# Performance work log

Hardware: AMD Instinct MI355X
Metric: run time of the kernel (lower is better)

## Reference

```python
import jax, jax.numpy as jnp
import numpy as np

FOCAL = 555.555
CROP_SIZE = 5
CROP_STEP = CROP_SIZE // 2  # 2
PADDING = CROP_SIZE        # 5
N_VIEWS = 16
IMG_SIZE = 400
N_POINTS = 65536


def _make_poses(n, radius=4.0, elev=-0.5):
    """NeRF-style camera-to-world matrices looking at the origin."""
    poses = []
    up = np.array([0.0, 0.0, 1.0], np.float64)
    for i in range(n):
        theta = 2.0 * np.pi * i / n
        eye = radius * np.array([np.cos(theta) * np.cos(elev),
                                 np.sin(theta) * np.cos(elev),
                                 np.sin(elev)], np.float64)
        z = eye / np.linalg.norm(eye)
        x = np.cross(up, z); x /= np.linalg.norm(x)
        y = np.cross(z, x)
        c2w = np.eye(4, dtype=np.float64)
        c2w[:3, 0] = x; c2w[:3, 1] = y; c2w[:3, 2] = z; c2w[:3, 3] = eye
        poses.append(c2w)
    return np.stack(poses).astype(np.float32)


def setup_inputs() -> dict:
    key = jax.random.key(0)
    k1, k2 = jax.random.split(key)
    points = jax.random.normal(k1, (N_POINTS, 3), jnp.float32)          # world pts near origin
    images = jax.random.uniform(k2, (N_VIEWS, IMG_SIZE, IMG_SIZE, 3), jnp.float32)
    poses = jnp.asarray(_make_poses(N_VIEWS))                            # [N,4,4]
    return {"points": points, "images": images, "poses": poses}


def _forward(points, images, poses):
    N, size = images.shape[0], images.shape[1]
    Hp = size + 2 * PADDING  # padded image side (grid normalized by this)
    dt = points.dtype

    # --- init-time camera setup (pose flip + inverse, intrinsics) ---
    flip = jnp.diag(jnp.array([-1.0, 1.0, 1.0, 1.0], dt))
    M = jnp.linalg.inv(poses @ flip)[:, :3, :]                           # [N,3,4] world->cam
    K = jnp.array([[FOCAL, 0.0, 0.5 * size],
                   [0.0, FOCAL, 0.5 * size],
                   [0.0, 0.0, 1.0]], dt)
    imgs = jnp.transpose(images, (0, 3, 1, 2))                           # [N,C,H,W]
    imgs = jnp.pad(imgs, ((0, 0), (0, 0), (PADDING, PADDING), (PADDING, PADDING)))  # zeros

    # --- projection ---
    P = points.shape[0]
    pts = jnp.concatenate([points, jnp.ones((P, 1), dt)], axis=1)        # [P,4]
    ps = jnp.einsum('ij,njk,pk->nip', K, M, pts)                         # [N,3,P]
    pix = jnp.clip((ps[:, :2] / ps[:, 2][:, None]) / size, 0.0, 1.0)     # [N,2,P] in [0,1]
    coord_norm = jnp.transpose(pix * 2.0 - 1.0, (0, 2, 1))               # [N,P,2]
    pixels = jnp.transpose(pix * size, (0, 2, 1))                        # [N,P,2] pixel units

    # --- 5x5 patch grid in padded-image pixel coords ---
    x = pixels[..., 0] + PADDING - CROP_STEP                             # [N,P]
    y = pixels[..., 1] + PADDING - CROP_STEP
    offs = jnp.arange(CROP_SIZE, dtype=dt)
    scale = (Hp - 1) / Hp  # grid_sample align_corners=True after v/Hp*2-1 normalization
    # NOTE: original stacks grid=[all_y, all_x, 0]: grid_sample x-coord (width) = all_y,
    # y-coord (height) = all_x. Rows vary along patch dim i, cols along patch dim j.
    rows = (x[:, :, None, None] + offs[None, None, :, None]) * scale     # [N,P,5,5]
    cols = (y[:, :, None, None] + offs[None, None, None, :]) * scale     # [N,P,5,5]

    def sample_view(img, r, c):  # img [C,Hp,Hp]; r,c [P,5,5]; bilinear, zeros padding
        r0f = jnp.floor(r); c0f = jnp.floor(c)
        wr = r - r0f; wc = c - c0f
        r0 = r0f.astype(jnp.int32); c0 = c0f.astype(jnp.int32)

        def gather(ri, ci):
            valid = ((ri >= 0) & (ri < Hp) & (ci >= 0) & (ci < Hp)).astype(img.dtype)
            v = img[:, jnp.clip(ri, 0, Hp - 1), jnp.clip(ci, 0, Hp - 1)]  # [C,P,5,5]
            return v * valid

        return (gather(r0, c0) * (1 - wr) * (1 - wc)
                + gather(r0, c0 + 1) * (1 - wr) * wc
                + gather(r0 + 1, c0) * wr * (1 - wc)
                + gather(r0 + 1, c0 + 1) * wr * wc)

    feats = jax.vmap(sample_view)(imgs, rows, cols)                      # [N,C,P,5,5]
    feats = jnp.transpose(feats, (2, 0, 1, 3, 4))                        # [P,N,C,5,5]
    return feats, coord_norm


def reference(points, images, poses):
    # Returns (feats [P,N,3,5,5], coord_norm [N,P,2]) -- the two tensors fed to the
    # external transformer in the original module.
    return _forward(points, images, poses)
```

## Files before the change

kernel.cpp:

```cpp
#include <hip/hip_runtime.h>

constexpr int   NPTS   = 65536;
constexpr int   NVIEWS = 16;
constexpr int   SZ     = 400;
constexpr int   PAD    = 5;
constexpr float FOCAL  = 555.555f;
constexpr float SCALE  = 409.0f / 410.0f;

constexpr long long FEATS_N = (long long)NPTS * NVIEWS * 3 * 25;

typedef float vfloat2 __attribute__((ext_vector_type(2)));

__global__ void setup_km(const float* __restrict__ poses, float* __restrict__ km) {
    int n = threadIdx.x;
    if (n >= NVIEWS) return;
    const float* A = poses + n * 16;
    float x0 = A[0], x1 = A[4], x2 = A[8];
    float y0 = A[1], y1 = A[5], y2 = A[9];
    float z0 = A[2], z1 = A[6], z2 = A[10];
    float t0 = A[3], t1 = A[7], t2 = A[11];

    float M0[4] = { -x0, -x1, -x2,  (x0 * t0 + x1 * t1 + x2 * t2) };
    float M1[4] = {  y0,  y1,  y2, -(y0 * t0 + y1 * t1 + y2 * t2) };
    float M2[4] = {  z0,  z1,  z2, -(z0 * t0 + z1 * t1 + z2 * t2) };

    const float f = FOCAL, cx = 0.5f * SZ;
    float* o = km + n * 12;
#pragma unroll
    for (int k = 0; k < 4; ++k) o[k]     = f * M0[k] + cx * M2[k];
#pragma unroll
    for (int k = 0; k < 4; ++k) o[4 + k] = f * M1[k] + cx * M2[k];
#pragma unroll
    for (int k = 0; k < 4; ++k) o[8 + k] = M2[k];
}

__device__ __forceinline__ void fetch3(const float* __restrict__ ib, int r, int c,
                                       float& a, float& b, float& d) {
    bool ok = ((unsigned)r < (unsigned)SZ) & ((unsigned)c < (unsigned)SZ);
    int rc = min(max(r, 0), SZ - 1);
    int cc = min(max(c, 0), SZ - 1);
    const float* q = ib + ((long long)rc * SZ + cc) * 3;
    float m = ok ? 1.0f : 0.0f;
    a = q[0] * m;
    b = q[1] * m;
    d = q[2] * m;
}

__global__ __launch_bounds__(256) void feats_kernel(const float* __restrict__ pts,
                                                    const float* __restrict__ imgs,
                                                    const float* __restrict__ km,
                                                    float* __restrict__ out) {
    unsigned b   = blockIdx.x;
    unsigned n   = (b & 7u) + 8u * ((b >> 3) & 1u);
    unsigned idx = (b >> 4) * 256u + threadIdx.x;
    unsigned p   = idx / 25u;
    unsigned ij  = idx % 25u;

    float px = pts[3 * p], py = pts[3 * p + 1], pz = pts[3 * p + 2];
    const float* k = km + n * 12;
    float psx = k[0] * px + k[1] * py + k[2]  * pz + k[3];
    float psy = k[4] * px + k[5] * py + k[6]  * pz + k[7];
    float psz = k[8] * px + k[9] * py + k[10] * pz + k[11];
    float inv = __builtin_amdgcn_rcpf(psz);
    float u = psx * inv * (1.0f / SZ);
    float v = psy * inv * (1.0f / SZ);
    u = fminf(fmaxf(u, 0.0f), 1.0f);
    v = fminf(fmaxf(v, 0.0f), 1.0f);
    float x = u * SZ + (float)(PAD - 2);
    float y = v * SZ + (float)(PAD - 2);

    int i = (int)(ij / 5u);
    int j = (int)(ij % 5u);

    float r  = (x + (float)i) * SCALE;
    float cc = (y + (float)j) * SCALE;
    float r0f = floorf(r);
    float c0f = floorf(cc);
    float wr = r - r0f;
    float wc = cc - c0f;
    int r0 = (int)r0f - PAD;
    int c0 = (int)c0f - PAD;

    const float* ib = imgs + (long long)n * (SZ * SZ * 3);
    float a00, b00, d00, a01, b01, d01, a10, b10, d10, a11, b11, d11;
    fetch3(ib, r0,     c0,     a00, b00, d00);
    fetch3(ib, r0,     c0 + 1, a01, b01, d01);
    fetch3(ib, r0 + 1, c0,     a10, b10, d10);
    fetch3(ib, r0 + 1, c0 + 1, a11, b11, d11);

    float w00 = (1.0f - wr) * (1.0f - wc);
    float w01 = (1.0f - wr) * wc;
    float w10 = wr * (1.0f - wc);
    float w11 = wr * wc;

    float o0 = w00 * a00 + w01 * a01 + w10 * a10 + w11 * a11;
    float o1 = w00 * b00 + w01 * b01 + w10 * b10 + w11 * b11;
    float o2 = w00 * d00 + w01 * d01 + w10 * d10 + w11 * d11;

    unsigned pn = p * 16u + n;
    float* ob = out + (long long)pn * 75 + ij;
    __builtin_nontemporal_store(o0, &ob[0]);
    __builtin_nontemporal_store(o1, &ob[25]);
    __builtin_nontemporal_store(o2, &ob[50]);
}

__global__ __launch_bounds__(256) void coord_kernel(const float* __restrict__ pts,
                                                    const float* __restrict__ km,
                                                    float* __restrict__ out2) {
    unsigned tid = blockIdx.x * 256u + threadIdx.x;
    unsigned p = tid & (NPTS - 1);
    unsigned n = tid >> 16;

    float px = pts[3 * p], py = pts[3 * p + 1], pz = pts[3 * p + 2];
    const float* k = km + n * 12;
    float psx = k[0] * px + k[1] * py + k[2]  * pz + k[3];
    float psy = k[4] * px + k[5] * py + k[6]  * pz + k[7];
    float psz = k[8] * px + k[9] * py + k[10] * pz + k[11];
    float inv = __builtin_amdgcn_rcpf(psz);
    float u = psx * inv * (1.0f / SZ);
    float v = psy * inv * (1.0f / SZ);
    u = fminf(fmaxf(u, 0.0f), 1.0f);
    v = fminf(fmaxf(v, 0.0f), 1.0f);

    vfloat2* o = (vfloat2*)out2;
    vfloat2 val = { 2.0f * u - 1.0f, 2.0f * v - 1.0f };
    __builtin_nontemporal_store(val, &o[tid]);
}

extern "C" void kernel_launch(void* const* d_in, const int* in_sizes, int n_in,
                              void* d_out, int out_size, void* d_ws, size_t ws_size,
                              hipStream_t stream) {
    const float* points = (const float*)d_in[0];
    const float* images = (const float*)d_in[1];
    const float* poses  = (const float*)d_in[2];
    float* out = (float*)d_out;
    float* km  = (float*)d_ws;

    setup_km<<<1, 64, 0, stream>>>(poses, km);

    feats_kernel<<<102400, 256, 0, stream>>>(points, images, km, out);

    coord_kernel<<<4096, 256, 0, stream>>>(points, km, out + FEATS_N);
}
```

Before: 433.0 us.

## Pre-pad images and stage per-point 6x6 patch in LDS for bilinear sampling

Adds a kernel that writes zero-padded copies of the images (row pitch 412) to workspace. The feats kernel now gives each 32-lane group one (point, view) pair: the group loads the covering 6-row patch into shared memory with float4 loads, then 25 lanes do the bilinear taps from LDS without bounds checks. This removes the per-tap clamping and scattered 4-byte global gathers. In exchange it adds a full image-padding pass, launches more blocks, leaves 7 of 32 lanes idle in the compute phase, and adds a block-wide barrier. The old path is kept as a fallback when the workspace is too small.

```diff
diff --git a/kernel.cpp b/kernel.cpp
--- a/kernel.cpp
+++ b/kernel.cpp
@@ -4,10 +4,14 @@
 constexpr int   NVIEWS = 16;
 constexpr int   SZ     = 400;
 constexpr int   PAD    = 5;
+constexpr int   HP     = 410;
+constexpr int   WP     = 412;
 constexpr float FOCAL  = 555.555f;
 constexpr float SCALE  = 409.0f / 410.0f;
 
 constexpr long long FEATS_N = (long long)NPTS * NVIEWS * 3 * 25;
+constexpr int PADIMG_FLOATS = NVIEWS * HP * WP * 3;
+constexpr int ROWB = WP * 3 * 4;
 
 typedef float vfloat2 __attribute__((ext_vector_type(2)));
 
@@ -34,27 +38,36 @@
     for (int k = 0; k < 4; ++k) o[8 + k] = M2[k];
 }
 
-__device__ __forceinline__ void fetch3(const float* __restrict__ ib, int r, int c,
-                                       float& a, float& b, float& d) {
-    bool ok = ((unsigned)r < (unsigned)SZ) & ((unsigned)c < (unsigned)SZ);
-    int rc = min(max(r, 0), SZ - 1);
-    int cc = min(max(c, 0), SZ - 1);
-    const float* q = ib + ((long long)rc * SZ + cc) * 3;
-    float m = ok ? 1.0f : 0.0f;
-    a = q[0] * m;
-    b = q[1] * m;
-    d = q[2] * m;
-}
-
-__global__ __launch_bounds__(256) void feats_kernel(const float* __restrict__ pts,
-                                                    const float* __restrict__ imgs,
-                                                    const float* __restrict__ km,
-                                                    float* __restrict__ out) {
-    unsigned b   = blockIdx.x;
-    unsigned n   = (b & 7u) + 8u * ((b >> 3) & 1u);
-    unsigned idx = (b >> 4) * 256u + threadIdx.x;
-    unsigned p   = idx / 25u;
-    unsigned ij  = idx % 25u;
+__global__ __launch_bounds__(256) void pad_kernel(const float* __restrict__ images,
+                                                  float* __restrict__ dst) {
+    unsigned idx = blockIdx.x * 256u + threadIdx.x;
+    constexpr unsigned TOT = (unsigned)NVIEWS * HP * WP;
+    if (idx >= TOT) return;
+    unsigned n   = idx / (unsigned)(HP * WP);
+    unsigned rem = idx - n * (unsigned)(HP * WP);
+    unsigned rr  = rem / (unsigned)WP;
+    unsigned cc  = rem - rr * (unsigned)WP;
+    float a = 0.0f, b = 0.0f, c = 0.0f;
+    int r = (int)rr - PAD, q = (int)cc - PAD;
+    if (r >= 0 && r < SZ && q >= 0 && q < SZ) {
+        const float* s = images + (((long long)n * SZ + r) * SZ + q) * 3;
+        a = s[0]; b = s[1]; c = s[2];
+    }
+    float* d = dst + (long long)idx * 3;
+    d[0] = a; d[1] = b; d[2] = c;
+}
+
+__global__ __launch_bounds__(256) void feats_coop(const float* __restrict__ pts,
+                                                  const float* __restrict__ imgpad,
+                                                  const float* __restrict__ km,
+                                                  float* __restrict__ out) {
+    __shared__ float lds[8 * 168];
+
+    unsigned b = blockIdx.x;
+    unsigned n = (b & 7u) + 8u * ((b >> 3) & 1u);
+    unsigned g = threadIdx.x >> 5;
+    unsigned l = threadIdx.x & 31u;
+    unsigned p = (b >> 4) * 8u + g;
 
     float px = pts[3 * p], py = pts[3 * p + 1], pz = pts[3 * p + 2];
     const float* k = km + n * 12;
@@ -69,47 +82,92 @@
     float x = u * SZ + (float)(PAD - 2);
     float y = v * SZ + (float)(PAD - 2);
 
-    int i = (int)(ij / 5u);
-    int j = (int)(ij % 5u);
-
-    float r  = (x + (float)i) * SCALE;
-    float cc = (y + (float)j) * SCALE;
-    float r0f = floorf(r);
-    float c0f = floorf(cc);
-    float wr = r - r0f;
-    float wc = cc - c0f;
-    int r0 = (int)r0f - PAD;
-    int c0 = (int)c0f - PAD;
-
-    const float* ib = imgs + (long long)n * (SZ * SZ * 3);
-    float a00, b00, d00, a01, b01, d01, a10, b10, d10, a11, b11, d11;
-    fetch3(ib, r0,     c0,     a00, b00, d00);
-    fetch3(ib, r0,     c0 + 1, a01, b01, d01);
-    fetch3(ib, r0 + 1, c0,     a10, b10, d10);
-    fetch3(ib, r0 + 1, c0 + 1, a11, b11, d11);
-
-    float w00 = (1.0f - wr) * (1.0f - wc);
-    float w01 = (1.0f - wr) * wc;
-    float w10 = wr * (1.0f - wc);
-    float w11 = wr * wc;
-
-    float o0 = w00 * a00 + w01 * a01 + w10 * a10 + w11 * a11;
-    float o1 = w00 * b00 + w01 * b01 + w10 * b10 + w11 * b11;
-    float o2 = w00 * d00 + w01 * d01 + w10 * d10 + w11 * d11;
-
-    unsigned pn = p * 16u + n;
-    float* ob = out + (long long)pn * 75 + ij;
-    __builtin_nontemporal_store(o0, &ob[0]);
-    __builtin_nontemporal_store(o1, &ob[25]);
-    __builtin_nontemporal_store(o2, &ob[50]);
-}
-
-__global__ __launch_bounds__(256) void coord_kernel(const float* __restrict__ pts,
+    int r_first = (int)floorf(x * SCALE);
+    int c_first = (int)floorf(y * SCALE);
+
+    unsigned colb = (unsigned)c_first * 12u;
+    unsigned base = colb & ~15u;
+    unsigned mis  = colb & 12u;
+
+    const char* gsrc = (const char*)imgpad
+                     + (size_t)n * ((size_t)HP * WP * 3 * 4)
+                     + (size_t)((unsigned)r_first * (unsigned)ROWB + base);
+    char* lbase = (char*)(lds + g * 168);
+
+    {
+        unsigned q  = l;
+        unsigned row = (q * 43u) >> 8;
+        unsigned ch  = q - 6u * row;
+        float4 val = *(const float4*)(gsrc + row * (unsigned)ROWB + ch * 16u);
+        *(float4*)(lbase + row * 112u + ch * 16u) = val;
+    }
+    if (l < 4u) {
+        unsigned q  = 32u + l;
+        unsigned row = (q * 43u) >> 8;
+        unsigned ch  = q - 6u * row;
+        float4 val = *(const float4*)(gsrc + row * (unsigned)ROWB + ch * 16u);
+        *(float4*)(lbase + row * 112u + ch * 16u) = val;
+    }
+    __syncthreads();
+
+    if (l < 25u) {
+        unsigned i = (l * 205u) >> 10;
+        unsigned j = l - 5u * i;
+
+        float r  = (x + (float)i) * SCALE;
+        float cc = (y + (float)j) * SCALE;
+        float r0f = floorf(r);
+        float c0f = floorf(cc);
+        float wr = r - r0f;
+        float wc = cc - c0f;
+        unsigned ri = (unsigned)((int)r0f - r_first);
+        unsigned cj = (unsigned)((int)c0f - c_first);
+
+        const float* row0 = (const float*)(lbase + ri * 112u + mis + cj * 12u);
+        const float* row1 = (const float*)((const char*)row0 + 112);
+        float a00 = row0[0], b00 = row0[1], d00 = row0[2];
+        float a01 = row0[3], b01 = row0[4], d01 = row0[5];
+        float a10 = row1[0], b10 = row1[1], d10 = row1[2];
+        float a11 = row1[3], b11 = row1[4], d11 = row1[5];
+
+        float w00 = (1.0f - wr) * (1.0f - wc);
+        float w01 = (1.0f - wr) * wc;
+        float w10 = wr * (1.0f - wc);
+        float w11 = wr * wc;
+
+        float o0 = w00 * a00 + w01 * a01 + w10 * a10 + w11 * a11;
+        float o1 = w00 * b00 + w01 * b01 + w10 * b10 + w11 * b11;
+        float o2 = w00 * d00 + w01 * d01 + w10 * d10 + w11 * d11;
+
+        unsigned pn = p * 16u + n;
+        float* ob = out + (long long)pn * 75 + l;
+        __builtin_nontemporal_store(o0, &ob[0]);
+        __builtin_nontemporal_store(o1, &ob[25]);
+        __builtin_nontemporal_store(o2, &ob[50]);
+    }
+}
+
+__device__ __forceinline__ void fetch3(const float* __restrict__ ib, int r, int c,
+                                       float& a, float& b, float& d) {
+    bool ok = ((unsigned)r < (unsigned)SZ) & ((unsigned)c < (unsigned)SZ);
+    int rc = min(max(r, 0), SZ - 1);
+    int cc = min(max(c, 0), SZ - 1);
+    const float* q = ib + ((long long)rc * SZ + cc) * 3;
+    float m = ok ? 1.0f : 0.0f;
+    a = q[0] * m;
+    b = q[1] * m;
+    d = q[2] * m;
+}
+
+__global__ __launch_bounds__(256) void feats_kernel(const float* __restrict__ pts,
+                                                    const float* __restrict__ imgs,
                                                     const float* __restrict__ km,
-                                                    float* __restrict__ out2) {
-    unsigned tid = blockIdx.x * 256u + threadIdx.x;
-    unsigned p = tid & (NPTS - 1);
-    unsigned n = tid >> 16;
+                                                    float* __restrict__ out) {
+    unsigned b   = blockIdx.x;
+    unsigned n   = (b & 7u) + 8u * ((b >> 3) & 1u);
+    unsigned idx = (b >> 4) * 256u + threadIdx.x;
+    unsigned p   = idx / 25u;
+    unsigned ij  = idx % 25u;
 
     float px = pts[3 * p], py = pts[3 * p + 1], pz = pts[3 * p + 2];
     const float* k = km + n * 12;
@@ -121,6 +179,61 @@
     float v = psy * inv * (1.0f / SZ);
     u = fminf(fmaxf(u, 0.0f), 1.0f);
     v = fminf(fmaxf(v, 0.0f), 1.0f);
+    float x = u * SZ + (float)(PAD - 2);
+    float y = v * SZ + (float)(PAD - 2);
+
+    int i = (int)(ij / 5u);
+    int j = (int)(ij % 5u);
+
+    float r  = (x + (float)i) * SCALE;
+    float cc = (y + (float)j) * SCALE;
+    float r0f = floorf(r);
+    float c0f = floorf(cc);
+    float wr = r - r0f;
+    float wc = cc - c0f;
+    int r0 = (int)r0f - PAD;
+    int c0 = (int)c0f - PAD;
+
+    const float* ib = imgs + (long long)n * (SZ * SZ * 3);
+    float a00, b00, d00, a01, b01, d01, a10, b10, d10, a11, b11, d11;
+    fetch3(ib, r0,     c0,     a00, b00, d00);
+    fetch3(ib, r0,     c0 + 1, a01, b01, d01);
+    fetch3(ib, r0 + 1, c0,     a10, b10, d10);
+    fetch3(ib, r0 + 1, c0 + 1, a11, b11, d11);
+
+    float w00 = (1.0f - wr) * (1.0f - wc);
+    float w01 = (1.0f - wr) * wc;
+    float w10 = wr * (1.0f - wc);
+    float w11 = wr * wc;
+
+    float o0 = w00 * a00 + w01 * a01 + w10 * a10 + w11 * a11;
+    float o1 = w00 * b00 + w01 * b01 + w10 * b10 + w11 * b11;
+    float o2 = w00 * d00 + w01 * d01 + w10 * d10 + w11 * d11;
+
+    unsigned pn = p * 16u + n;
+    float* ob = out + (long long)pn * 75 + ij;
+    __builtin_nontemporal_store(o0, &ob[0]);
+    __builtin_nontemporal_store(o1, &ob[25]);
+    __builtin_nontemporal_store(o2, &ob[50]);
+}
+
+__global__ __launch_bounds__(256) void coord_kernel(const float* __restrict__ pts,
+                                                    const float* __restrict__ km,
+                                                    float* __restrict__ out2) {
+    unsigned tid = blockIdx.x * 256u + threadIdx.x;
+    unsigned p = tid & (NPTS - 1);
+    unsigned n = tid >> 16;
+
+    float px = pts[3 * p], py = pts[3 * p + 1], pz = pts[3 * p + 2];
+    const float* k = km + n * 12;
+    float psx = k[0] * px + k[1] * py + k[2]  * pz + k[3];
+    float psy = k[4] * px + k[5] * py + k[6]  * pz + k[7];
+    float psz = k[8] * px + k[9] * py + k[10] * pz + k[11];
+    float inv = __builtin_amdgcn_rcpf(psz);
+    float u = psx * inv * (1.0f / SZ);
+    float v = psy * inv * (1.0f / SZ);
+    u = fminf(fmaxf(u, 0.0f), 1.0f);
+    v = fminf(fmaxf(v, 0.0f), 1.0f);
 
     vfloat2* o = (vfloat2*)out2;
     vfloat2 val = { 2.0f * u - 1.0f, 2.0f * v - 1.0f };
@@ -134,11 +247,25 @@
     const float* images = (const float*)d_in[1];
     const float* poses  = (const float*)d_in[2];
     float* out = (float*)d_out;
-    float* km  = (float*)d_ws;
-
-    setup_km<<<1, 64, 0, stream>>>(poses, km);
-
-    feats_kernel<<<102400, 256, 0, stream>>>(points, images, km, out);
-
-    coord_kernel<<<4096, 256, 0, stream>>>(points, km, out + FEATS_N);
-}
+
+    const size_t ws_needed = ((size_t)PADIMG_FLOATS + 256) * 4;
+
+    if (ws_size >= ws_needed) {
+        float* imgpad = (float*)d_ws;
+        float* km     = imgpad + PADIMG_FLOATS;
+
+        setup_km<<<1, 64, 0, stream>>>(poses, km);
+
+        constexpr unsigned PADTOT = (unsigned)NVIEWS * HP * WP;
+        pad_kernel<<<(PADTOT + 255) / 256, 256, 0, stream>>>(images, imgpad);
+
+        feats_coop<<<131072, 256, 0, stream>>>(points, imgpad, km, out);
+
+        coord_kernel<<<4096, 256, 0, stream>>>(points, km, out + FEATS_N);
+    } else {
+        float* km = (float*)d_ws;
+        setup_km<<<1, 64, 0, stream>>>(poses, km);
+        feats_kernel<<<102400, 256, 0, stream>>>(points, images, km, out);
+        coord_kernel<<<4096, 256, 0, stream>>>(points, km, out + FEATS_N);
+    }
+}
```

New measurement: 456.1 us. +5.3%, slower.

## Stage per-point 6x7 image patch in LDS via float4 loads before bilinear sampling

Applied to the files above, without the earlier changes.

Each group of 32 threads now serves one (point, view) pair. The group cooperatively loads the 6-row by 7-pixel RGB neighbourhood into shared memory with aligned float4 loads, zero-filling out-of-bounds parts, and after a barrier 25 lanes do bilinear interpolation from LDS. This replaces 12 scattered scalar global loads per output with about 36 vector loads per 25 outputs. In exchange 7 of every 32 lanes sit idle in the compute phase, a block-wide barrier is added, and the grid grows to 131072 blocks.

```diff
diff --git a/kernel.cpp b/kernel.cpp
--- a/kernel.cpp
+++ b/kernel.cpp
@@ -8,6 +8,7 @@
 constexpr float SCALE  = 409.0f / 410.0f;
 
 constexpr long long FEATS_N = (long long)NPTS * NVIEWS * 3 * 25;
+constexpr int ROWB = SZ * 3 * 4;
 
 typedef float vfloat2 __attribute__((ext_vector_type(2)));
 
@@ -34,27 +35,17 @@
     for (int k = 0; k < 4; ++k) o[8 + k] = M2[k];
 }
 
-__device__ __forceinline__ void fetch3(const float* __restrict__ ib, int r, int c,
-                                       float& a, float& b, float& d) {
-    bool ok = ((unsigned)r < (unsigned)SZ) & ((unsigned)c < (unsigned)SZ);
-    int rc = min(max(r, 0), SZ - 1);
-    int cc = min(max(c, 0), SZ - 1);
-    const float* q = ib + ((long long)rc * SZ + cc) * 3;
-    float m = ok ? 1.0f : 0.0f;
-    a = q[0] * m;
-    b = q[1] * m;
-    d = q[2] * m;
-}
+__global__ __launch_bounds__(256) void feats_coop(const float* __restrict__ pts,
+                                                  const float* __restrict__ imgs,
+                                                  const float* __restrict__ km,
+                                                  float* __restrict__ out) {
+    __shared__ float lds[8 * 168];
 
-__global__ __launch_bounds__(256) void feats_kernel(const float* __restrict__ pts,
-                                                    const float* __restrict__ imgs,
-                                                    const float* __restrict__ km,
-                                                    float* __restrict__ out) {
-    unsigned b   = blockIdx.x;
-    unsigned n   = (b & 7u) + 8u * ((b >> 3) & 1u);
-    unsigned idx = (b >> 4) * 256u + threadIdx.x;
-    unsigned p   = idx / 25u;
-    unsigned ij  = idx % 25u;
+    unsigned b = blockIdx.x;
+    unsigned n = (b & 7u) + 8u * ((b >> 3) & 1u);
+    unsigned g = threadIdx.x >> 5;
+    unsigned l = threadIdx.x & 31u;
+    unsigned p = (b >> 4) * 8u + g;
 
     float px = pts[3 * p], py = pts[3 * p + 1], pz = pts[3 * p + 2];
     const float* k = km + n * 12;
@@ -69,39 +60,77 @@
     float x = u * SZ + (float)(PAD - 2);
     float y = v * SZ + (float)(PAD - 2);
 
-    int i = (int)(ij / 5u);
-    int j = (int)(ij % 5u);
+    int r_first = (int)floorf(x * SCALE);
+    int c_first = (int)floorf(y * SCALE);
 
-    float r  = (x + (float)i) * SCALE;
-    float cc = (y + (float)j) * SCALE;
-    float r0f = floorf(r);
-    float c0f = floorf(cc);
-    float wr = r - r0f;
-    float wc = cc - c0f;
-    int r0 = (int)r0f - PAD;
-    int c0 = (int)c0f - PAD;
+    int colb = (c_first - PAD) * 12;
+    int base = colb & ~15;
+    unsigned mis = (unsigned)(colb & 12);
 
-    const float* ib = imgs + (long long)n * (SZ * SZ * 3);
-    float a00, b00, d00, a01, b01, d01, a10, b10, d10, a11, b11, d11;
-    fetch3(ib, r0,     c0,     a00, b00, d00);
-    fetch3(ib, r0,     c0 + 1, a01, b01, d01);
-    fetch3(ib, r0 + 1, c0,     a10, b10, d10);
-    fetch3(ib, r0 + 1, c0 + 1, a11, b11, d11);
+    const char* ibase = (const char*)imgs + (size_t)n * (SZ * SZ * 3 * 4);
+    char* lbase = (char*)(lds + g * 168);
 
-    float w00 = (1.0f - wr) * (1.0f - wc);
-    float w01 = (1.0f - wr) * wc;
-    float w10 = wr * (1.0f - wc);
-    float w11 = wr * wc;
+    {
+        unsigned q   = l;
+        unsigned row = (q * 43u) >> 8;
+        unsigned ch  = q - 6u * row;
+        int row_orig = r_first - PAD + (int)row;
+        int sbyte    = base + (int)(ch * 16u);
+        float4 val = {0.0f, 0.0f, 0.0f, 0.0f};
+        if (((unsigned)row_orig < (unsigned)SZ) & ((unsigned)sbyte < (unsigned)ROWB))
+            val = *(const float4*)(ibase + (size_t)((unsigned)row_orig * (unsigned)ROWB
+                                                    + (unsigned)sbyte));
+        *(float4*)(lbase + row * 112u + ch * 16u) = val;
+    }
+    if (l < 4u) {
+        unsigned q   = 32u + l;
+        unsigned row = (q * 43u) >> 8;
+        unsigned ch  = q - 6u * row;
+        int row_orig = r_first - PAD + (int)row;
+        int sbyte    = base + (int)(ch * 16u);
+        float4 val = {0.0f, 0.0f, 0.0f, 0.0f};
+        if (((unsigned)row_orig < (unsigned)SZ) & ((unsigned)sbyte < (unsigned)ROWB))
+            val = *(const float4*)(ibase + (size_t)((unsigned)row_orig * (unsigned)ROWB
+                                                    + (unsigned)sbyte));
+        *(float4*)(lbase + row * 112u + ch * 16u) = val;
+    }
+    __syncthreads();
 
-    float o0 = w00 * a00 + w01 * a01 + w10 * a10 + w11 * a11;
-    float o1 = w00 * b00 + w01 * b01 + w10 * b10 + w11 * b11;
-    float o2 = w00 * d00 + w01 * d01 + w10 * d10 + w11 * d11;
+    if (l < 25u) {
+        unsigned i = (l * 205u) >> 10;
+        unsigned j = l - 5u * i;
 
-    unsigned pn = p * 16u + n;
-    float* ob = out + (long long)pn * 75 + ij;
-    __builtin_nontemporal_store(o0, &ob[0]);
-    __builtin_nontemporal_store(o1, &ob[25]);
-    __builtin_nontemporal_store(o2, &ob[50]);
+        float r  = (x + (float)i) * SCALE;
+        float cc = (y + (float)j) * SCALE;
+        float r0f = floorf(r);
+        float c0f = floorf(cc);
+        float wr = r - r0f;
+        float wc = cc - c0f;
+        unsigned ri = (unsigned)((int)r0f - r_first);
+        unsigned cj = (unsigned)((int)c0f - c_first);
+
+        const float* row0 = (const float*)(lbase + ri * 112u + mis + cj * 12u);
+        const float* row1 = (const float*)((const char*)row0 + 112);
+        float a00 = row0[0], b00 = row0[1], d00 = row0[2];
+        float a01 = row0[3], b01 = row0[4], d01 = row0[5];
+        float a10 = row1[0], b10 = row1[1], d10 = row1[2];
+        float a11 = row1[3], b11 = row1[4], d11 = row1[5];
+
+        float w00 = (1.0f - wr) * (1.0f - wc);
+        float w01 = (1.0f - wr) * wc;
+        float w10 = wr * (1.0f - wc);
+        float w11 = wr * wc;
+
+        float o0 = w00 * a00 + w01 * a01 + w10 * a10 + w11 * a11;
+        float o1 = w00 * b00 + w01 * b01 + w10 * b10 + w11 * b11;
+        float o2 = w00 * d00 + w01 * d01 + w10 * d10 + w11 * d11;
+
+        unsigned pn = p * 16u + n;
+        float* ob = out + (long long)pn * 75 + l;
+        __builtin_nontemporal_store(o0, &ob[0]);
+        __builtin_nontemporal_store(o1, &ob[25]);
+        __builtin_nontemporal_store(o2, &ob[50]);
+    }
 }
 
 __global__ __launch_bounds__(256) void coord_kernel(const float* __restrict__ pts,
@@ -138,7 +167,7 @@
 
     setup_km<<<1, 64, 0, stream>>>(poses, km);
 
-    feats_kernel<<<102400, 256, 0, stream>>>(points, images, km, out);
+    feats_coop<<<131072, 256, 0, stream>>>(points, images, km, out);
 
     coord_kernel<<<4096, 256, 0, stream>>>(points, km, out + FEATS_N);
 }
```

Result: slower. 445.7 us (+2.9%).

## Stage per-point feats in LDS and write contiguous float4 nontemporal stores

Applied to the files above, without the earlier changes.

Restructures the feats kernel so each block handles 8 points, with 32 threads per point (25 active) looping over all 16 views. Results go to shared memory, then the block writes its 9600-float output slab as contiguous float4 nontemporal stores instead of strided scalar stores. This aims at better write coalescing and reuses the point load across views. In exchange, 7 of 32 lanes sit idle, blocks are far fewer with a serial view loop, and 38KB of LDS per block may limit occupancy.

```diff
diff --git a/kernel.cpp b/kernel.cpp
--- a/kernel.cpp
+++ b/kernel.cpp
@@ -10,6 +10,7 @@
 constexpr long long FEATS_N = (long long)NPTS * NVIEWS * 3 * 25;
 
 typedef float vfloat2 __attribute__((ext_vector_type(2)));
+typedef float vfloat4 __attribute__((ext_vector_type(4)));
 
 __global__ void setup_km(const float* __restrict__ poses, float* __restrict__ km) {
     int n = threadIdx.x;
@@ -46,62 +47,78 @@
     d = q[2] * m;
 }
 
-__global__ __launch_bounds__(256) void feats_kernel(const float* __restrict__ pts,
-                                                    const float* __restrict__ imgs,
-                                                    const float* __restrict__ km,
-                                                    float* __restrict__ out) {
-    unsigned b   = blockIdx.x;
-    unsigned n   = (b & 7u) + 8u * ((b >> 3) & 1u);
-    unsigned idx = (b >> 4) * 256u + threadIdx.x;
-    unsigned p   = idx / 25u;
-    unsigned ij  = idx % 25u;
+__global__ __launch_bounds__(256) void feats_dense(const float* __restrict__ pts,
+                                                   const float* __restrict__ imgs,
+                                                   const float* __restrict__ km,
+                                                   float* __restrict__ out) {
+    __attribute__((aligned(16))) __shared__ float obuf[8 * 1200];
+
+    unsigned b = blockIdx.x;
+    unsigned g = threadIdx.x >> 5;
+    unsigned l = threadIdx.x & 31u;
+    unsigned p = b * 8u + g;
 
     float px = pts[3 * p], py = pts[3 * p + 1], pz = pts[3 * p + 2];
-    const float* k = km + n * 12;
-    float psx = k[0] * px + k[1] * py + k[2]  * pz + k[3];
-    float psy = k[4] * px + k[5] * py + k[6]  * pz + k[7];
-    float psz = k[8] * px + k[9] * py + k[10] * pz + k[11];
-    float inv = __builtin_amdgcn_rcpf(psz);
-    float u = psx * inv * (1.0f / SZ);
-    float v = psy * inv * (1.0f / SZ);
-    u = fminf(fmaxf(u, 0.0f), 1.0f);
-    v = fminf(fmaxf(v, 0.0f), 1.0f);
-    float x = u * SZ + (float)(PAD - 2);
-    float y = v * SZ + (float)(PAD - 2);
 
-    int i = (int)(ij / 5u);
-    int j = (int)(ij % 5u);
+    unsigned i = (l * 205u) >> 10;
+    unsigned j = l - 5u * i;
+    bool active = (l < 25u);
+    float fi = (float)i, fj = (float)j;
 
-    float r  = (x + (float)i) * SCALE;
-    float cc = (y + (float)j) * SCALE;
-    float r0f = floorf(r);
-    float c0f = floorf(cc);
-    float wr = r - r0f;
-    float wc = cc - c0f;
-    int r0 = (int)r0f - PAD;
-    int c0 = (int)c0f - PAD;
+    float* oisl = obuf + g * 1200u;
 
-    const float* ib = imgs + (long long)n * (SZ * SZ * 3);
-    float a00, b00, d00, a01, b01, d01, a10, b10, d10, a11, b11, d11;
-    fetch3(ib, r0,     c0,     a00, b00, d00);
-    fetch3(ib, r0,     c0 + 1, a01, b01, d01);
-    fetch3(ib, r0 + 1, c0,     a10, b10, d10);
-    fetch3(ib, r0 + 1, c0 + 1, a11, b11, d11);
+    for (unsigned n = 0; n < (unsigned)NVIEWS; ++n) {
+        const float* k = km + n * 12u;
+        float psx = k[0] * px + k[1] * py + k[2]  * pz + k[3];
+        float psy = k[4] * px + k[5] * py + k[6]  * pz + k[7];
+        float psz = k[8] * px + k[9] * py + k[10] * pz + k[11];
+        float inv = __builtin_amdgcn_rcpf(psz);
+        float u = psx * inv * (1.0f / SZ);
+        float v = psy * inv * (1.0f / SZ);
+        u = fminf(fmaxf(u, 0.0f), 1.0f);
+        v = fminf(fmaxf(v, 0.0f), 1.0f);
+        float x = u * SZ + (float)(PAD - 2);
+        float y = v * SZ + (float)(PAD - 2);
 
-    float w00 = (1.0f - wr) * (1.0f - wc);
-    float w01 = (1.0f - wr) * wc;
-    float w10 = wr * (1.0f - wc);
-    float w11 = wr * wc;
+        if (active) {
+            float r  = (x + fi) * SCALE;
+            float cc = (y + fj) * SCALE;
+            float r0f = floorf(r);
+            float c0f = floorf(cc);
+            float wr = r - r0f;
+            float wc = cc - c0f;
+            int r0 = (int)r0f - PAD;
+            int c0 = (int)c0f - PAD;
 
-    float o0 = w00 * a00 + w01 * a01 + w10 * a10 + w11 * a11;
-    float o1 = w00 * b00 + w01 * b01 + w10 * b10 + w11 * b11;
-    float o2 = w00 * d00 + w01 * d01 + w10 * d10 + w11 * d11;
+            const float* ib = imgs + (long long)n * (SZ * SZ * 3);
+            float a00, b00, d00, a01, b01, d01, a10, b10, d10, a11, b11, d11;
+            fetch3(ib, r0,     c0,     a00, b00, d00);
+            fetch3(ib, r0,     c0 + 1, a01, b01, d01);
+            fetch3(ib, r0 + 1, c0,     a10, b10, d10);
+            fetch3(ib, r0 + 1, c0 + 1, a11, b11, d11);
 
-    unsigned pn = p * 16u + n;
-    float* ob = out + (long long)pn * 75 + ij;
-    __builtin_nontemporal_store(o0, &ob[0]);
-    __builtin_nontemporal_store(o1, &ob[25]);
-    __builtin_nontemporal_store(o2, &ob[50]);
+            float w00 = (1.0f - wr) * (1.0f - wc);
+            float w01 = (1.0f - wr) * wc;
+            float w10 = wr * (1.0f - wc);
+            float w11 = wr * wc;
+
+            float o0 = w00 * a00 + w01 * a01 + w10 * a10 + w11 * a11;
+            float o1 = w00 * b00 + w01 * b01 + w10 * b10 + w11 * b11;
+            float o2 = w00 * d00 + w01 * d01 + w10 * d10 + w11 * d11;
+
+            unsigned base = n * 75u + l;
+            oisl[base]       = o0;
+            oisl[base + 25u] = o1;
+            oisl[base + 50u] = o2;
+        }
+    }
+    __syncthreads();
+
+    const vfloat4* src = (const vfloat4*)obuf;
+    vfloat4* dst = (vfloat4*)(out + (size_t)b * 9600u);
+    unsigned t = threadIdx.x;
+    for (unsigned q = t; q < 2400u; q += 256u)
+        __builtin_nontemporal_store(src[q], &dst[q]);
 }
 
 __global__ __launch_bounds__(256) void coord_kernel(const float* __restrict__ pts,
@@ -138,7 +155,7 @@
 
     setup_km<<<1, 64, 0, stream>>>(poses, km);
 
-    feats_kernel<<<102400, 256, 0, stream>>>(points, images, km, out);
+    feats_dense<<<8192, 256, 0, stream>>>(points, images, km, out);
 
     coord_kernel<<<4096, 256, 0, stream>>>(points, km, out + FEATS_N);
 }
```

Measured after the change: 429.3 us. About the same (-0.8%).
